# Kernel optimization log

Hardware: AMD Instinct MI355X
Metric: run time of the kernel (lower is better)

Reference implementation:

```python
import jax, jax.numpy as jnp
import numpy as np

N = 100000   # ntoken / num nodes
D = 256      # ninp
E = 3200000  # num edges
BN_EPS = 1e-5


def gcn_conv(x, W, b, src, dst, num_nodes):
    """PyG GCNConv: add self-loops, symmetric deg normalization, aggregate at dst."""
    loop = jnp.arange(num_nodes, dtype=src.dtype)
    src = jnp.concatenate([src, loop])
    dst = jnp.concatenate([dst, loop])
    deg = jax.ops.segment_sum(jnp.ones_like(dst, dtype=x.dtype), dst,
                              num_segments=num_nodes)
    dinv = jnp.where(deg > 0, jax.lax.rsqrt(deg), 0.0)
    norm = dinv[src] * dinv[dst]          # [E+N]
    xw = x @ W                            # [N, out]
    msg = xw[src] * norm[:, None]         # gather + scale
    out = jax.ops.segment_sum(msg, dst, num_segments=num_nodes)
    return out + b


def batch_norm(x, gamma, beta):
    # training-mode BatchNorm1d over node dim (biased variance)
    mean = jnp.mean(x, axis=0)
    var = jnp.mean((x - mean) ** 2, axis=0)
    return gamma * (x - mean) * jax.lax.rsqrt(var + BN_EPS) + beta


def setup_inputs() -> dict:
    key = jax.random.key(0)
    ks = jax.random.split(key, 5)
    edge_index = jax.random.randint(ks[0], (2, E), 0, N, dtype=jnp.int64)
    emb_weight = jax.random.normal(ks[1], (N, D), dtype=jnp.float32) * 0.05
    W1 = jax.random.normal(ks[2], (D, 2 * D), dtype=jnp.float32) * 0.05
    b1 = jnp.zeros((2 * D,), dtype=jnp.float32)
    W2 = jax.random.normal(ks[3], (2 * D, D), dtype=jnp.float32) * 0.05
    b2 = jnp.zeros((D,), dtype=jnp.float32)
    gamma = jnp.ones((D,), dtype=jnp.float32)
    beta = jnp.zeros((D,), dtype=jnp.float32)
    return {"edge_index": edge_index, "emb_weight": emb_weight,
            "W1": W1, "b1": b1, "W2": W2, "b2": b2,
            "gamma": gamma, "beta": beta}


def reference(edge_index, emb_weight, W1, b1, W2, b2, gamma, beta):
    src, dst = edge_index[0], edge_index[1]
    h = gcn_conv(emb_weight, W1, b1, src, dst, N)   # [N, 2D]
    # dropout is identity in eval / deterministic reference
    h = gcn_conv(h, W2, b2, src, dst, N)            # [N, D]
    return batch_norm(h, gamma, beta)
```

## Files before the change

### kernel.cpp

```cpp
#include <hip/hip_runtime.h>
#include <hip/hip_fp16.h>
#include <math.h>

#define DIM   256
#define DIM4  64
#define DIMH2 64
#define BN_EPS 1e-5f

#define NPB      256
#define MAXBUCK  512
#define CAP      13312

typedef __attribute__((ext_vector_type(8))) _Float16 half8;
typedef __attribute__((ext_vector_type(4))) float f32x4;

__device__ __forceinline__ unsigned h2u(__half2 h) { return __builtin_bit_cast(unsigned, h); }
__device__ __forceinline__ __half2 u2h(unsigned u) { return __builtin_bit_cast(__half2, u); }

__global__ void k_deg_init(int* __restrict__ deg, int N) {
    int i = blockIdx.x * blockDim.x + threadIdx.x;
    if (i < N) deg[i] = 1;
}

__global__ void k_deg_count(const int* __restrict__ dst, int* __restrict__ deg, int E) {
    for (int e = blockIdx.x * blockDim.x + threadIdx.x; e < E; e += gridDim.x * blockDim.x) {
        atomicAdd(&deg[dst[e]], 1);
    }
}

__global__ void k_dinv(const int* __restrict__ deg, float* __restrict__ dinv, int N) {
    int i = blockIdx.x * blockDim.x + threadIdx.x;
    if (i < N) dinv[i] = rsqrtf((float)deg[i]);
}

__global__ __launch_bounds__(256) void k_tohalf(const float4* __restrict__ in,
                                                uint2* __restrict__ outh, int n4) {
    for (int i = blockIdx.x * blockDim.x + threadIdx.x; i < n4; i += gridDim.x * blockDim.x) {
        float4 v = in[i];
        uint2 o;
        o.x = h2u(__halves2half2(__float2half_rn(v.x), __float2half_rn(v.y)));
        o.y = h2u(__halves2half2(__float2half_rn(v.z), __float2half_rn(v.w)));
        outh[i] = o;
    }
}

__global__ void k_scan_partial(const int* __restrict__ deg, int* __restrict__ part, int N) {
    __shared__ int sh[256];
    int base = blockIdx.x * 1024 + threadIdx.x * 4;
    int s = 0;
#pragma unroll
    for (int q = 0; q < 4; ++q) {
        int i = base + q;
        if (i < N) s += deg[i] - 1;
    }
    sh[threadIdx.x] = s;
    __syncthreads();
    for (int off = 128; off > 0; off >>= 1) {
        if (threadIdx.x < off) sh[threadIdx.x] += sh[threadIdx.x + off];
        __syncthreads();
    }
    if (threadIdx.x == 0) part[blockIdx.x] = sh[0];
}

__global__ void k_scan_offsets(int* __restrict__ part, int* __restrict__ rowstart, int nb, int N) {
    int run = 0;
    for (int i = 0; i < nb; ++i) { int v = part[i]; part[i] = run; run += v; }
    rowstart[N] = run;
}

__global__ void k_scan_write(const int* __restrict__ deg, const int* __restrict__ part,
                             int* __restrict__ rowstart, int N) {
    __shared__ int sh[256];
    int base = blockIdx.x * 1024 + threadIdx.x * 4;
    int v[4]; int s = 0;
#pragma unroll
    for (int q = 0; q < 4; ++q) {
        int i = base + q;
        v[q] = (i < N) ? deg[i] - 1 : 0;
        s += v[q];
    }
    sh[threadIdx.x] = s;
    __syncthreads();
    if (threadIdx.x == 0) {
        int run = part[blockIdx.x];
        for (int t = 0; t < 256; ++t) { int x = sh[t]; sh[t] = run; run += x; }
    }
    __syncthreads();
    int run = sh[threadIdx.x];
#pragma unroll
    for (int q = 0; q < 4; ++q) {
        int i = base + q;
        if (i < N) { rowstart[i] = run; run += v[q]; }
    }
}

__global__ void k_bucket_init(const int* __restrict__ rowstart, int* __restrict__ gcur,
                              int N, int nbuck) {
    int b = blockIdx.x * blockDim.x + threadIdx.x;
    if (b < nbuck) {
        int n = b * NPB;
        gcur[b] = rowstart[n < N ? n : N];
    }
}

__global__ __launch_bounds__(256) void k_binfill(const int* __restrict__ src,
                                                 const int* __restrict__ dst,
                                                 int* __restrict__ gcur,
                                                 uint2* __restrict__ stage,
                                                 int E, int nbuck) {
    __shared__ int hist[MAXBUCK];
    __shared__ int base[MAXBUCK];
    int tid = threadIdx.x;
    int chunk = (E + gridDim.x - 1) / gridDim.x;
    int e0 = blockIdx.x * chunk;
    int e1 = min(E, e0 + chunk);
    for (int b = tid; b < nbuck; b += 256) hist[b] = 0;
    __syncthreads();
    for (int e = e0 + tid; e < e1; e += 256)
        atomicAdd(&hist[dst[e] >> 8], 1);
    __syncthreads();
    for (int b = tid; b < nbuck; b += 256)
        base[b] = atomicAdd(&gcur[b], hist[b]);
    __syncthreads();
    for (int b = tid; b < nbuck; b += 256) hist[b] = 0;
    __syncthreads();
    for (int e = e0 + tid; e < e1; e += 256) {
        int d = dst[e];
        int bk = d >> 8;
        int p = base[bk] + atomicAdd(&hist[bk], 1);
        stage[p] = make_uint2((unsigned)src[e], (unsigned)d);
    }
}

__global__ __launch_bounds__(256) void k_csrbuild(const uint2* __restrict__ stage,
                                                  const int* __restrict__ rowstart,
                                                  int* __restrict__ col, int N) {
    __shared__ int cur[NPB];
    __shared__ int lcol[CAP];
    int b   = blockIdx.x;
    int tid = threadIdx.x;
    int n0  = b << 8;
    int n1  = min(N, n0 + NPB);
    int r0  = rowstart[n0];
    int r1  = rowstart[n1];
    int cnt = r1 - r0;
    if (n0 + tid < n1) cur[tid] = rowstart[n0 + tid] - r0;
    __syncthreads();
    if (cnt <= CAP) {
        for (int i = tid; i < cnt; i += 256) {
            uint2 rec = stage[r0 + i];
            int p = atomicAdd(&cur[(int)rec.y - n0], 1);
            lcol[p] = (int)rec.x;
        }
        __syncthreads();
        for (int i = tid; i < cnt; i += 256)
            col[r0 + i] = lcol[i];
    } else {
        for (int i = tid; i < cnt; i += 256) {
            uint2 rec = stage[r0 + i];
            int p = atomicAdd(&cur[(int)rec.y - n0], 1);
            col[r0 + p] = (int)rec.x;
        }
    }
}

__global__ __launch_bounds__(256) void k_agg_h2h(const uint2* __restrict__ xh,
                                                 const float* __restrict__ dinv,
                                                 const int* __restrict__ rowstart,
                                                 const int* __restrict__ col,
                                                 uint2* __restrict__ outh,
                                                 float* __restrict__ rs, int N, int writeRs) {
    int wave = (blockIdx.x * blockDim.x + threadIdx.x) >> 6;
    int lane = threadIdx.x & 63;
    if (wave >= N) return;
    float di = dinv[wave];
    uint2 xraw = xh[(size_t)wave * DIMH2 + lane];
    float2 f0 = __half22float2(u2h(xraw.x));
    float2 f1 = __half22float2(u2h(xraw.y));
    float ax = di * f0.x, ay = di * f0.y, az = di * f1.x, aw = di * f1.y;
    float sd = 0.f;
    int p = rowstart[wave], e = rowstart[wave + 1];
    if (p < e) {
        int j = col[p]; float dj = dinv[j];
        for (++p; p < e; ++p) {
            int jn = col[p]; float djn = dinv[jn];
            uint2 raw = xh[(size_t)j * DIMH2 + lane];
            float2 v0 = __half22float2(u2h(raw.x));
            float2 v1 = __half22float2(u2h(raw.y));
            ax += dj * v0.x; ay += dj * v0.y; az += dj * v1.x; aw += dj * v1.y;
            sd += dj;
            j = jn; dj = djn;
        }
        uint2 raw = xh[(size_t)j * DIMH2 + lane];
        float2 v0 = __half22float2(u2h(raw.x));
        float2 v1 = __half22float2(u2h(raw.y));
        ax += dj * v0.x; ay += dj * v0.y; az += dj * v1.x; aw += dj * v1.y;
        sd += dj;
    }
    uint2 o;
    o.x = h2u(__halves2half2(__float2half_rn(di * ax), __float2half_rn(di * ay)));
    o.y = h2u(__halves2half2(__float2half_rn(di * az), __float2half_rn(di * aw)));
    outh[(size_t)wave * DIMH2 + lane] = o;
    if (writeRs && lane == 0) rs[wave] = di * (sd + di);
}

__global__ void k_wct(const float* __restrict__ W1, const float* __restrict__ W2,
                      _Float16* __restrict__ WcT) {
    int i = blockIdx.x, j = threadIdx.x;
    float acc = 0.f;
    for (int k = 0; k < 2 * DIM; ++k) acc += W1[i * 2 * DIM + k] * W2[k * DIM + j];
    WcT[(size_t)j * DIM + i] = (_Float16)acc;
}

__global__ void k_cvec(const float* __restrict__ b1, const float* __restrict__ W2,
                       float* __restrict__ cvec) {
    int j = threadIdx.x;
    float acc = 0.f;
    for (int k = 0; k < 2 * DIM; ++k) acc += b1[k] * W2[k * DIM + j];
    cvec[j] = acc;
}

#define GBM 128
#define GBN 128
#define ASTR 40

__global__ __launch_bounds__(256) void k_gemm_mfma(const _Float16* __restrict__ Ah,
                                                   const _Float16* __restrict__ BTh,
                                                   const float* __restrict__ rs,
                                                   const float* __restrict__ cvec,
                                                   const float* __restrict__ b2,
                                                   float* __restrict__ C, int N) {
    __shared__ _Float16 As[GBM][ASTR];
    __shared__ _Float16 Bs[GBN][ASTR];
    int tid  = threadIdx.x;
    int row0 = blockIdx.x * GBM;
    int col0 = blockIdx.y * GBN;
    int w    = tid >> 6;
    int lane = tid & 63;
    int wr   = (w >> 1) * 64;
    int wc   = (w & 1) * 64;
    int lr   = lane & 15;
    int kg   = lane >> 4;

    f32x4 acc[4][4];
#pragma unroll
    for (int i = 0; i < 4; ++i)
#pragma unroll
        for (int j = 0; j < 4; ++j) acc[i][j] = (f32x4)0.f;

    int sr = tid >> 2;
    int sc = (tid & 3) * 8;

    for (int k0 = 0; k0 < DIM; k0 += 32) {
        __syncthreads();
#pragma unroll
        for (int q = 0; q < 2; ++q) {
            int r  = sr + q * 64;
            int gr = row0 + r;
            half8 av = (half8)(_Float16)0.f;
            if (gr < N)
                av = *reinterpret_cast<const half8*>(&Ah[(size_t)gr * DIM + k0 + sc]);
            *reinterpret_cast<half8*>(&As[r][sc]) = av;
            half8 bv = *reinterpret_cast<const half8*>(&BTh[(size_t)(col0 + r) * DIM + k0 + sc]);
            *reinterpret_cast<half8*>(&Bs[r][sc]) = bv;
        }
        __syncthreads();

        half8 af[4], bf[4];
#pragma unroll
        for (int mm = 0; mm < 4; ++mm)
            af[mm] = *reinterpret_cast<const half8*>(&As[wr + mm * 16 + lr][kg * 8]);
#pragma unroll
        for (int nn = 0; nn < 4; ++nn)
            bf[nn] = *reinterpret_cast<const half8*>(&Bs[wc + nn * 16 + lr][kg * 8]);
#pragma unroll
        for (int mm = 0; mm < 4; ++mm)
#pragma unroll
            for (int nn = 0; nn < 4; ++nn)
                acc[mm][nn] = __builtin_amdgcn_mfma_f32_16x16x32_f16(af[mm], bf[nn],
                                                                     acc[mm][nn], 0, 0, 0);
    }

#pragma unroll
    for (int mm = 0; mm < 4; ++mm) {
        int rbase = row0 + wr + mm * 16 + kg * 4;
#pragma unroll
        for (int reg = 0; reg < 4; ++reg) {
            int r = rbase + reg;
            if (r < N) {
                float rv = rs[r];
#pragma unroll
                for (int nn = 0; nn < 4; ++nn) {
                    int c = col0 + wc + nn * 16 + lr;
                    C[(size_t)r * DIM + c] = acc[mm][nn][reg] + rv * cvec[c] + b2[c];
                }
            }
        }
    }
}

__global__ void k_bnzero(float* __restrict__ p) {
    p[threadIdx.x] = 0.f;
}

__global__ __launch_bounds__(256) void k_bnstats(const float* __restrict__ h,
                                                 float* __restrict__ sum,
                                                 float* __restrict__ sq, int N) {
    int ch = threadIdx.x;
    float s = 0.f, ss = 0.f;
    for (int r = blockIdx.x; r < N; r += gridDim.x) {
        float v = h[r * DIM + ch];
        s += v; ss += v * v;
    }
    atomicAdd(&sum[ch], s);
    atomicAdd(&sq[ch], ss);
}

__global__ void k_bnfinal(const float* __restrict__ sum, const float* __restrict__ sq,
                          const float* __restrict__ gamma, const float* __restrict__ beta,
                          float* __restrict__ scale, float* __restrict__ shift, int N) {
    int ch = threadIdx.x;
    float invN = 1.0f / (float)N;
    float mean = sum[ch] * invN;
    float var = sq[ch] * invN - mean * mean;
    float inv = rsqrtf(var + BN_EPS);
    float sc = gamma[ch] * inv;
    scale[ch] = sc;
    shift[ch] = beta[ch] - mean * sc;
}

__global__ __launch_bounds__(256) void k_bnnorm(float4* __restrict__ out,
                                                const float4* __restrict__ scale,
                                                const float4* __restrict__ shift, int n4) {
    for (int i = blockIdx.x * blockDim.x + threadIdx.x; i < n4; i += gridDim.x * blockDim.x) {
        int j = i & (DIM4 - 1);
        float4 v = out[i];
        float4 sc = scale[j];
        float4 sh = shift[j];
        v.x = v.x * sc.x + sh.x;
        v.y = v.y * sc.y + sh.y;
        v.z = v.z * sc.z + sh.z;
        v.w = v.w * sc.w + sh.w;
        out[i] = v;
    }
}

extern "C" void kernel_launch(void* const* d_in, const int* in_sizes, int n_in,
                              void* d_out, int out_size, void* d_ws, size_t ws_size,
                              hipStream_t stream) {
    const int* ei        = (const int*)d_in[0];
    const float* emb     = (const float*)d_in[1];
    const float* W1      = (const float*)d_in[2];
    const float* b1      = (const float*)d_in[3];
    const float* W2      = (const float*)d_in[4];
    const float* b2      = (const float*)d_in[5];
    const float* gamma   = (const float*)d_in[6];
    const float* beta    = (const float*)d_in[7];

    const int E = in_sizes[0] / 2;
    const int N = in_sizes[1] / DIM;
    const int* src = ei;
    const int* dst = ei + E;
    const int nbuck = (N + NPB - 1) / NPB;

    char* w = (char*)d_ws;
    size_t off = 0;
    auto alloc = [&](size_t bytes) -> void* {
        off = (off + 255) & ~(size_t)255;
        void* p = w + off;
        off += bytes;
        return p;
    };
    int*      deg      = (int*)     alloc((size_t)N * 4);
    float*    dinv     = (float*)   alloc((size_t)N * 4);
    int*      rowstart = (int*)     alloc((size_t)(N + 1) * 4);
    int*      gcur     = (int*)     alloc((size_t)(nbuck + 1) * 4);
    int*      part     = (int*)     alloc(1024);
    int*      csr_col  = (int*)     alloc((size_t)E * 4);
    uint2*    stage    = (uint2*)   alloc((size_t)E * 8);
    float*    rs       = (float*)   alloc((size_t)N * 4);
    uint2*    agg2h    = (uint2*)   alloc((size_t)N * DIM * 2);
    _Float16* WcTh     = (_Float16*)alloc((size_t)DIM * DIM * 2);
    float*    cvec     = (float*)   alloc(DIM * 4);
    float*    bnsum    = (float*)   alloc(2 * DIM * 4);
    float*    bnscale  = (float*)   alloc(2 * DIM * 4);

    uint2* xh    = (uint2*)d_out;
    uint2* agg1h = (uint2*)((char*)d_out + (size_t)N * DIM * 2);
    float* out   = (float*)d_out;

    const int nb1024 = (N + 1023) / 1024;

    k_deg_init<<<(N + 255) / 256, 256, 0, stream>>>(deg, N);
    k_deg_count<<<2048, 256, 0, stream>>>(dst, deg, E);
    k_dinv<<<(N + 255) / 256, 256, 0, stream>>>(deg, dinv, N);

    k_tohalf<<<2048, 256, 0, stream>>>((const float4*)emb, xh, N * DIM4);

    k_scan_partial<<<nb1024, 256, 0, stream>>>(deg, part, N);
    k_scan_offsets<<<1, 1, 0, stream>>>(part, rowstart, nb1024, N);
    k_scan_write<<<nb1024, 256, 0, stream>>>(deg, part, rowstart, N);
    k_bucket_init<<<(nbuck + 255) / 256, 256, 0, stream>>>(rowstart, gcur, N, nbuck);
    k_binfill<<<256, 256, 0, stream>>>(src, dst, gcur, stage, E, nbuck);
    k_csrbuild<<<nbuck, 256, 0, stream>>>(stage, rowstart, csr_col, N);

    k_agg_h2h<<<(N + 3) / 4, 256, 0, stream>>>(xh, dinv, rowstart, csr_col, agg1h, rs, N, 1);
    k_agg_h2h<<<(N + 3) / 4, 256, 0, stream>>>(agg1h, dinv, rowstart, csr_col, agg2h, rs, N, 0);

    k_wct<<<DIM, DIM, 0, stream>>>(W1, W2, WcTh);
    k_cvec<<<1, DIM, 0, stream>>>(b1, W2, cvec);

    dim3 ggrid((N + GBM - 1) / GBM, DIM / GBN);
    k_gemm_mfma<<<ggrid, 256, 0, stream>>>((const _Float16*)agg2h, WcTh, rs, cvec, b2, out, N);

    k_bnzero<<<1, 512, 0, stream>>>(bnsum);
    k_bnstats<<<512, 256, 0, stream>>>(out, bnsum, bnsum + DIM, N);
    k_bnfinal<<<1, DIM, 0, stream>>>(bnsum, bnsum + DIM, gamma, beta,
                                     bnscale, bnscale + DIM, N);
    k_bnnorm<<<2048, 256, 0, stream>>>((float4*)out, (const float4*)bnscale,
                                       (const float4*)(bnscale + DIM), N * DIM4);
}
```

Baseline: 1.091 ms.

## Prescale features by dinv to drop per-edge dinv gathers in aggregation

Source features are pre-multiplied by dinv when converted to half, and the first aggregation writes its output scaled by di^2. Each aggregation pass then sums neighbor rows without a per-edge dinv gather or multiply. The row-sum term rs moves into a separate lane-parallel kernel, and the aggregation loop is unrolled by four so more gathers are in flight. The cost is one extra launch plus another pass over col and dinv, and fp16 values now carry the scaled magnitudes, which changes rounding.

New measurement: 1.076 ms. No clear change (-1.3%).

```diff
diff --git a/kernel.cpp b/kernel.cpp
--- a/kernel.cpp
+++ b/kernel.cpp
@@ -33,13 +33,15 @@
     if (i < N) dinv[i] = rsqrtf((float)deg[i]);
 }
 
-__global__ __launch_bounds__(256) void k_tohalf(const float4* __restrict__ in,
-                                                uint2* __restrict__ outh, int n4) {
+__global__ __launch_bounds__(256) void k_tohalf_u(const float4* __restrict__ in,
+                                                  const float* __restrict__ dinv,
+                                                  uint2* __restrict__ outh, int n4) {
     for (int i = blockIdx.x * blockDim.x + threadIdx.x; i < n4; i += gridDim.x * blockDim.x) {
+        float d = dinv[i >> 6];
         float4 v = in[i];
         uint2 o;
-        o.x = h2u(__halves2half2(__float2half_rn(v.x), __float2half_rn(v.y)));
-        o.y = h2u(__halves2half2(__float2half_rn(v.z), __float2half_rn(v.w)));
+        o.x = h2u(__halves2half2(__float2half_rn(d * v.x), __float2half_rn(d * v.y)));
+        o.y = h2u(__halves2half2(__float2half_rn(d * v.z), __float2half_rn(d * v.w)));
         outh[i] = o;
     }
 }
@@ -164,44 +166,65 @@
     }
 }
 
-__global__ __launch_bounds__(256) void k_agg_h2h(const uint2* __restrict__ xh,
-                                                 const float* __restrict__ dinv,
-                                                 const int* __restrict__ rowstart,
-                                                 const int* __restrict__ col,
-                                                 uint2* __restrict__ outh,
-                                                 float* __restrict__ rs, int N, int writeRs) {
+__global__ __launch_bounds__(256) void k_rs(const float* __restrict__ dinv,
+                                            const int* __restrict__ rowstart,
+                                            const int* __restrict__ col,
+                                            float* __restrict__ rs, int N) {
     int wave = (blockIdx.x * blockDim.x + threadIdx.x) >> 6;
     int lane = threadIdx.x & 63;
     if (wave >= N) return;
+    int s = rowstart[wave], e = rowstart[wave + 1];
+    float sd = 0.f;
+    for (int p = s + lane; p < e; p += 64) sd += dinv[col[p]];
+#pragma unroll
+    for (int off = 32; off > 0; off >>= 1) sd += __shfl_xor(sd, off);
+    if (lane == 0) {
+        float di = dinv[wave];
+        rs[wave] = di * (sd + di);
+    }
+}
+
+__global__ __launch_bounds__(256) void k_agg_u(const uint2* __restrict__ uh,
+                                               const float* __restrict__ dinv,
+                                               const int* __restrict__ rowstart,
+                                               const int* __restrict__ col,
+                                               uint2* __restrict__ outh,
+                                               int N, int squareDi) {
+    int wave = (blockIdx.x * blockDim.x + threadIdx.x) >> 6;
+    int lane = threadIdx.x & 63;
+    if (wave >= N) return;
+    uint2 uself = uh[(size_t)wave * DIMH2 + lane];
+    float2 f0 = __half22float2(u2h(uself.x));
+    float2 f1 = __half22float2(u2h(uself.y));
+    float ax = f0.x, ay = f0.y, az = f1.x, aw = f1.y;
+    int p = rowstart[wave], e = rowstart[wave + 1];
+    for (; p + 3 < e; p += 4) {
+        int j0 = col[p], j1 = col[p + 1], j2 = col[p + 2], j3 = col[p + 3];
+        uint2 r0 = uh[(size_t)j0 * DIMH2 + lane];
+        uint2 r1 = uh[(size_t)j1 * DIMH2 + lane];
+        uint2 r2 = uh[(size_t)j2 * DIMH2 + lane];
+        uint2 r3 = uh[(size_t)j3 * DIMH2 + lane];
+        float2 a0 = __half22float2(u2h(r0.x)), b0 = __half22float2(u2h(r0.y));
+        float2 a1 = __half22float2(u2h(r1.x)), b1 = __half22float2(u2h(r1.y));
+        float2 a2 = __half22float2(u2h(r2.x)), b2 = __half22float2(u2h(r2.y));
+        float2 a3 = __half22float2(u2h(r3.x)), b3 = __half22float2(u2h(r3.y));
+        ax += (a0.x + a1.x) + (a2.x + a3.x);
+        ay += (a0.y + a1.y) + (a2.y + a3.y);
+        az += (b0.x + b1.x) + (b2.x + b3.x);
+        aw += (b0.y + b1.y) + (b2.y + b3.y);
+    }
+    for (; p < e; ++p) {
+        int j = col[p];
+        uint2 r = uh[(size_t)j * DIMH2 + lane];
+        float2 a = __half22float2(u2h(r.x)), b = __half22float2(u2h(r.y));
+        ax += a.x; ay += a.y; az += b.x; aw += b.y;
+    }
     float di = dinv[wave];
-    uint2 xraw = xh[(size_t)wave * DIMH2 + lane];
-    float2 f0 = __half22float2(u2h(xraw.x));
-    float2 f1 = __half22float2(u2h(xraw.y));
-    float ax = di * f0.x, ay = di * f0.y, az = di * f1.x, aw = di * f1.y;
-    float sd = 0.f;
-    int p = rowstart[wave], e = rowstart[wave + 1];
-    if (p < e) {
-        int j = col[p]; float dj = dinv[j];
-        for (++p; p < e; ++p) {
-            int jn = col[p]; float djn = dinv[jn];
-            uint2 raw = xh[(size_t)j * DIMH2 + lane];
-            float2 v0 = __half22float2(u2h(raw.x));
-            float2 v1 = __half22float2(u2h(raw.y));
-            ax += dj * v0.x; ay += dj * v0.y; az += dj * v1.x; aw += dj * v1.y;
-            sd += dj;
-            j = jn; dj = djn;
-        }
-        uint2 raw = xh[(size_t)j * DIMH2 + lane];
-        float2 v0 = __half22float2(u2h(raw.x));
-        float2 v1 = __half22float2(u2h(raw.y));
-        ax += dj * v0.x; ay += dj * v0.y; az += dj * v1.x; aw += dj * v1.y;
-        sd += dj;
-    }
+    float s = squareDi ? di * di : di;
     uint2 o;
-    o.x = h2u(__halves2half2(__float2half_rn(di * ax), __float2half_rn(di * ay)));
-    o.y = h2u(__halves2half2(__float2half_rn(di * az), __float2half_rn(di * aw)));
+    o.x = h2u(__halves2half2(__float2half_rn(s * ax), __float2half_rn(s * ay)));
+    o.y = h2u(__halves2half2(__float2half_rn(s * az), __float2half_rn(s * aw)));
     outh[(size_t)wave * DIMH2 + lane] = o;
-    if (writeRs && lane == 0) rs[wave] = di * (sd + di);
 }
 
 __global__ void k_wct(const float* __restrict__ W1, const float* __restrict__ W2,
@@ -395,7 +418,7 @@
     k_deg_count<<<2048, 256, 0, stream>>>(dst, deg, E);
     k_dinv<<<(N + 255) / 256, 256, 0, stream>>>(deg, dinv, N);
 
-    k_tohalf<<<2048, 256, 0, stream>>>((const float4*)emb, xh, N * DIM4);
+    k_tohalf_u<<<2048, 256, 0, stream>>>((const float4*)emb, dinv, xh, N * DIM4);
 
     k_scan_partial<<<nb1024, 256, 0, stream>>>(deg, part, N);
     k_scan_offsets<<<1, 1, 0, stream>>>(part, rowstart, nb1024, N);
@@ -404,8 +427,10 @@
     k_binfill<<<256, 256, 0, stream>>>(src, dst, gcur, stage, E, nbuck);
     k_csrbuild<<<nbuck, 256, 0, stream>>>(stage, rowstart, csr_col, N);
 
-    k_agg_h2h<<<(N + 3) / 4, 256, 0, stream>>>(xh, dinv, rowstart, csr_col, agg1h, rs, N, 1);
-    k_agg_h2h<<<(N + 3) / 4, 256, 0, stream>>>(agg1h, dinv, rowstart, csr_col, agg2h, rs, N, 0);
+    k_rs<<<(N + 3) / 4, 256, 0, stream>>>(dinv, rowstart, csr_col, rs, N);
+
+    k_agg_u<<<(N + 3) / 4, 256, 0, stream>>>(xh, dinv, rowstart, csr_col, agg1h, N, 1);
+    k_agg_u<<<(N + 3) / 4, 256, 0, stream>>>(agg1h, dinv, rowstart, csr_col, agg2h, N, 0);
 
     k_wct<<<DIM, DIM, 0, stream>>>(W1, W2, WcTh);
     k_cvec<<<1, DIM, 0, stream>>>(b1, W2, cvec);
```
